# Kernel optimization log

Hardware: AMD Instinct MI355X
Metric: run time of the kernel (lower is better)

Reference implementation:

```python
import jax, jax.numpy as jnp
import numpy as np
from jax import lax

NEG = -1e30  # safe -inf surrogate (avoids inf-inf NaNs under vjp)


def setup_inputs() -> dict:
    key = jax.random.key(0)
    k1, k2, k3, k4 = jax.random.split(key, 4)
    B, T, U, V = 8, 128, 64, 1024
    acts = jax.random.normal(k1, (B, T, U + 1, V), dtype=jnp.float32)
    # labels in [1, V): blank (0) never appears in target sequences
    labels = jax.random.randint(k2, (B, U), 1, V, dtype=jnp.int32)
    act_lens = jax.random.randint(k3, (B,), T // 2, T + 1, dtype=jnp.int32)
    label_lens = jax.random.randint(k4, (B,), U // 2, U + 1, dtype=jnp.int32)
    return {"acts": acts, "labels": labels, "act_lens": act_lens, "label_lens": label_lens}


def _rnnt_costs(acts, labels, act_lens, label_lens, blank=0):
    """Per-example negative log-likelihood of the RNNT alignment lattice.
    acts: (B, T, U+1, V) logits (warp_rnnt applies log_softmax internally).
    """
    B, T, U1, V = acts.shape
    U = U1 - 1
    lp = jax.nn.log_softmax(acts, axis=-1)
    lp_blank = lp[..., blank]                                        # (B, T, U+1)
    lab = jnp.broadcast_to(labels[:, None, :, None], (B, T, U, 1))
    lp_label = jnp.take_along_axis(lp[:, :, :U, :], lab, axis=3)[..., 0]  # (B, T, U)
    # mask label emissions beyond each example's label length
    umask = jnp.arange(U)[None, :] < label_lens[:, None]             # (B, U)
    lp_label = jnp.where(umask[:, None, :], lp_label, NEG)

    def compute_row(fb, lt):
        # fb: (B, U+1) alpha[t-1, u] + lp_blank[t-1, u] (the "from below" term)
        # lt: (B, U)   label log-probs at time t
        # new[u] = logaddexp(fb[u], new[u-1] + lt[u-1])  -- sequential in u
        def u_step(carry, x):
            fb_u, lt_u = x
            new = jnp.logaddexp(fb_u, carry + lt_u)
            return new, new
        _, rest = lax.scan(u_step, fb[:, 0], (fb[:, 1:].T, lt.T))    # (U, B)
        return jnp.concatenate([fb[:, 0:1], rest.T], axis=1)         # (B, U+1)

    # t = 0 row: alpha[0,0] = 0; only label transitions along u
    fb0 = jnp.concatenate([jnp.zeros((B, 1), acts.dtype), jnp.full((B, U), NEG, acts.dtype)], axis=1)
    row0 = compute_row(fb0, lp_label[:, 0, :])

    def t_step(prev_row, x):
        lpb_prev, lt = x
        row = compute_row(prev_row + lpb_prev, lt)
        return row, row

    xs = (jnp.moveaxis(lp_blank[:, :-1, :], 0, 1),   # (T-1, B, U+1)
          jnp.moveaxis(lp_label[:, 1:, :], 0, 1))    # (T-1, B, U)
    _, rows = lax.scan(t_step, row0, xs)             # (T-1, B, U+1)
    alphas = jnp.concatenate([row0[None], rows], axis=0)  # (T, B, U+1)

    b = jnp.arange(B)
    tl = act_lens - 1
    final = alphas[tl, b, label_lens] + lp_blank[b, tl, label_lens]
    return -final                                     # (B,)


def reference(acts, labels, act_lens, label_lens):
    # matches torch module defaults: size_average=False, blank_label=0
    costs = _rnnt_costs(acts, labels, act_lens, label_lens, blank=0)
    return jnp.sum(costs).reshape(1)
```

## Files before the change

kernel.cpp:

```cpp
#include <hip/hip_runtime.h>

#define LN2F 0.6931471805599453f

#define B_   8
#define T_   128
#define U_   64
#define U1_  65
#define V_   1024
#define ROWS_ (B_*T_*U1_)
#define NDIAG_ 224
#define DS_    66
#define PACKB_ (NDIAG_*DS_)
#define COL0N_ 224
#define NWAVES_ 8192
#define K1_BLOCKS_ 2048

typedef float f32x4 __attribute__((ext_vector_type(4)));

__device__ __forceinline__ float shr1_f32(float x) {
  return __int_as_float(__builtin_amdgcn_update_dpp(
      0, __float_as_int(x), 0x138, 0xf, 0xf, true));
}

__device__ __forceinline__ float wave_fmax_dpp(float x) {
#define DPPM_(ctrl) { int t_ = __builtin_amdgcn_update_dpp(                  \
      __float_as_int(x), __float_as_int(x), (ctrl), 0xf, 0xf, false);        \
    x = fmaxf(x, __int_as_float(t_)); }
  DPPM_(0x111) DPPM_(0x112) DPPM_(0x114) DPPM_(0x118)
  DPPM_(0x142) DPPM_(0x143)
#undef DPPM_
  return __int_as_float(__builtin_amdgcn_readlane(__float_as_int(x), 63));
}

__device__ __forceinline__ float wave_fsum_dpp(float x) {
#define DPPA_(ctrl) { int t_ = __builtin_amdgcn_update_dpp(                  \
      0, __float_as_int(x), (ctrl), 0xf, 0xf, true);                         \
    x += __int_as_float(t_); }
  DPPA_(0x111) DPPA_(0x112) DPPA_(0x114) DPPA_(0x118)
  DPPA_(0x142) DPPA_(0x143)
#undef DPPA_
  return __int_as_float(__builtin_amdgcn_readlane(__float_as_int(x), 63));
}

__device__ __forceinline__ int wave_max_bexp(float a, float i0) {
  int e  = (int)((__float_as_uint(a)  >> 23) & 0xffu);
  int e2 = (int)((__float_as_uint(i0) >> 23) & 0xffu);
  e = max(e, e2);
  int t;
  t = __builtin_amdgcn_update_dpp(e, e, 0x111, 0xf, 0xf, false); e = max(e, t);
  t = __builtin_amdgcn_update_dpp(e, e, 0x112, 0xf, 0xf, false); e = max(e, t);
  t = __builtin_amdgcn_update_dpp(e, e, 0x114, 0xf, 0xf, false); e = max(e, t);
  t = __builtin_amdgcn_update_dpp(e, e, 0x118, 0xf, 0xf, false); e = max(e, t);
  t = __builtin_amdgcn_update_dpp(e, e, 0x142, 0xf, 0xf, false); e = max(e, t);
  t = __builtin_amdgcn_update_dpp(e, e, 0x143, 0xf, 0xf, false); e = max(e, t);
  return __builtin_amdgcn_readlane(e, 63);
}

__global__ __launch_bounds__(256) void k1_linsoftmax(
    const float* __restrict__ acts, const int* __restrict__ labels,
    const int* __restrict__ label_lens,
    float2* __restrict__ pack, float2* __restrict__ col0, int* __restrict__ cnt) {
  const int lane = threadIdx.x & 63;
  const int wid  = blockIdx.x * 4 + (threadIdx.x >> 6);
  if (wid == 0 && lane == 0) *cnt = 0;

  for (int row = wid; row < ROWS_; row += NWAVES_) {
    const int b   = row / (T_ * U1_);
    const int rem = row - b * (T_ * U1_);
    const int t   = rem / U1_;
    const int u   = rem - t * U1_;
    const float* __restrict__ p = acts + (size_t)row * V_;

    int ll_ = 0; float labv = 0.0f;
    if (lane == 0 && u < U_) {
      ll_  = label_lens[b];
      labv = p[labels[b * U_ + u]];
    }

    f32x4 v0 = *(const f32x4*)(p +   0 + lane * 4);
    f32x4 v1 = *(const f32x4*)(p + 256 + lane * 4);
    f32x4 v2 = *(const f32x4*)(p + 512 + lane * 4);
    f32x4 v3 = *(const f32x4*)(p + 768 + lane * 4);

    float ml = fmaxf(fmaxf(fmaxf(v0.x, v0.y), fmaxf(v0.z, v0.w)),
               fmaxf(fmaxf(fmaxf(v1.x, v1.y), fmaxf(v1.z, v1.w)),
               fmaxf(fmaxf(fmaxf(v2.x, v2.y), fmaxf(v2.z, v2.w)),
                     fmaxf(fmaxf(v3.x, v3.y), fmaxf(v3.z, v3.w)))));
    float m = wave_fmax_dpp(ml);

    float e00 = __expf(v0.x - m);
    float sl = e00          + __expf(v0.y - m) + __expf(v0.z - m) + __expf(v0.w - m)
             + __expf(v1.x - m) + __expf(v1.y - m) + __expf(v1.z - m) + __expf(v1.w - m)
             + __expf(v2.x - m) + __expf(v2.y - m) + __expf(v2.z - m) + __expf(v2.w - m)
             + __expf(v3.x - m) + __expf(v3.y - m) + __expf(v3.z - m) + __expf(v3.w - m);
    float s = wave_fsum_dpp(sl);

    if (lane == 0) {
      float rs = 1.0f / s;
      float pb = e00 * rs;
      float2* pk = pack + (size_t)b * PACKB_;
      if (u == 0) {
        float pl0 = __expf(labv - m) * rs;
        col0[b * COL0N_ + (t + 1)] = make_float2(pb, pl0);
        pk[(size_t)(t + 1) * DS_ + 1].x = pl0;
      } else {
        pk[(size_t)(t + u) * DS_ + u].y = pb;
        if (u < U_) {
          float plv = (u < ll_) ? (__expf(labv - m) * rs) : 0.0f;
          pk[(size_t)(t + u + 1) * DS_ + (u + 1)].x = plv;
        }
      }
    }
  }
}

__global__ __launch_bounds__(64) void k2_alpha(
    const float2* __restrict__ pack, const float2* __restrict__ col0,
    const int* __restrict__ act_lens, const int* __restrict__ label_lens,
    float* __restrict__ costs, int* __restrict__ cnt, float* __restrict__ out) {
  __shared__ float2 c0_s[COL0N_];
  const int b  = (int)blockIdx.x;
  const int l  = (int)threadIdx.x;

  {
    const float2* src = col0 + (size_t)b * COL0N_;
    #pragma unroll
    for (int k = 0; k < 4; ++k) {
      int i = k * 64 + l;
      if (i < COL0N_) {
        float2 v = src[i];
        bool ok = (i >= 1) && (i <= T_);
        c0_s[i] = ok ? v : make_float2(0.0f, 0.0f);
      }
    }
  }

  const int tl = act_lens[b] - 1;
  const int ll = label_lens[b];
  const int u  = l + 1;
  const int tcap = (u == ll) ? tl : 0x7fffffff;

  const float2* __restrict__ pku = pack + (size_t)b * PACKB_ + u;

  float a = 0.0f;
  float i0 = (l == 0) ? 1.0f : 0.0f;
  float fin = 0.0f, pbc = 0.0f;
  int   S = 0, Ecap = 0;
  int   t_ = -u;

  float2 pA[16], pB[16], pC[16], pD[16];
  float2 cA[16], cB[16], cC[16], cD[16];

#define LOADP(P, C, DB) do {                                             \
    const float2* q_ = pku + (size_t)(DB) * DS_;                         \
    _Pragma("unroll")                                                    \
    for (int j = 0; j < 16; ++j) (P)[j] = q_[(size_t)j * DS_];           \
    _Pragma("unroll")                                                    \
    for (int j = 0; j < 16; ++j) (C)[j] = c0_s[(DB) + j];                \
  } while (0)

#define RENORM() do {                                                    \
    int eS_ = wave_max_bexp(a, i0);                                      \
    int sh_ = min(167 - eS_, 126);     \
    S += sh_;                                                            \
    float sc_ = ldexpf(1.0f, sh_);                                       \
    a *= sc_; i0 *= sc_;                                                 \
  } while (0)

#define COMPUTE8(P, C, JO) do {                                          \
    _Pragma("unroll")                                                    \
    for (int jj = 0; jj < 8; ++jj) {                                     \
      const int j = (JO) + jj;                                           \
      t_ += 1;                                                           \
      float shin = shr1_f32(a);                                          \
      float inj  = i0 * (C)[j].y;                                        \
      float anew = fmaf(a, pbc, fmaf(shin, (P)[j].x, inj));              \
      bool valid = ((unsigned)t_ < (unsigned)T_);                        \
      a = valid ? anew : 0.0f;                \
      bool cap = (t_ == tcap);                                           \
      fin  = cap ? a : fin;                                              \
      Ecap = cap ? S : Ecap;                                             \
      i0 *= (C)[j].x;                                                    \
      pbc = (P)[j].y;                                                    \
    }                                                                    \
  } while (0)

  LOADP(pA, cA, 1);
  LOADP(pB, cB, 17);
  LOADP(pC, cC, 33);
  LOADP(pD, cD, 49);

  #pragma unroll 1
  for (int it4 = 0; it4 < 3; ++it4) {
    if (it4 > 0) RENORM();
    COMPUTE8(pA, cA, 0);
    RENORM();
    COMPUTE8(pA, cA, 8);
    if (it4 < 2) LOADP(pA, cA, 64 * it4 + 65);

    RENORM();
    COMPUTE8(pB, cB, 0);
    RENORM();
    COMPUTE8(pB, cB, 8);
    if (it4 < 2) LOADP(pB, cB, 64 * it4 + 81);

    RENORM();
    COMPUTE8(pC, cC, 0);
    RENORM();
    COMPUTE8(pC, cC, 8);
    if (it4 < 2) LOADP(pC, cC, 64 * it4 + 97);

    RENORM();
    COMPUTE8(pD, cD, 0);
    RENORM();
    COMPUTE8(pD, cD, 8);
    if (it4 < 2) LOADP(pD, cD, 64 * it4 + 113);
  }
#undef LOADP
#undef RENORM
#undef COMPUTE8

  if (u == ll) {
    float pblast = pack[(size_t)b * PACKB_ + (size_t)(tl + ll) * DS_ + ll].y;
    float lg = __log2f(fin) - (float)Ecap + __log2f(pblast);
    costs[b] = -lg * LN2F;
  }

  __threadfence();
  if (l == 0) {
    int old = atomicAdd(cnt, 1);
    if (old == B_ - 1) {
      __threadfence();
      volatile const float* vc = costs;
      float s = 0.0f;
      #pragma unroll
      for (int i = 0; i < B_; ++i) s += vc[i];
      out[0] = s;
    }
  }
}

extern "C" void kernel_launch(void* const* d_in, const int* in_sizes, int n_in,
                              void* d_out, int out_size, void* d_ws, size_t ws_size,
                              hipStream_t stream) {
  const float* acts       = (const float*)d_in[0];
  const int*   labels     = (const int*)d_in[1];
  const int*   act_lens   = (const int*)d_in[2];
  const int*   label_lens = (const int*)d_in[3];

  float2* pack  = (float2*)d_ws;
  float2* col0  = pack + (size_t)B_ * PACKB_;
  float*  costs = (float*)(col0 + (size_t)B_ * COL0N_);
  int*    cnt   = (int*)(costs + B_);

  k1_linsoftmax<<<K1_BLOCKS_, 256, 0, stream>>>(acts, labels, label_lens, pack, col0, cnt);
  k2_alpha<<<B_, 64, 0, stream>>>(pack, col0, act_lens, label_lens, costs, cnt, (float*)d_out);
}
```

Measured before the change: 57.34 us.

## Transpose packed lattice probs to per-lane rows in bf16 and prefetch all upfront

The lattice probability workspace is re-laid out so each lane's diagonal sequence is contiguous (one 256-entry row per u), and each label/blank pair is packed into a single 32-bit word of two bf16 values. The alpha kernel then issues all 13 groups of 16-byte vector loads up front instead of strided per-step float2 loads in four rotating buffers. This is meant to remove the latency-bound strided gathers on the single-wave serial recursion. The cost is lower precision (bf16 probabilities), which may change the loss beyond tolerance, and much higher register pressure.

```diff
diff --git a/kernel.cpp b/kernel.cpp
--- a/kernel.cpp
+++ b/kernel.cpp
@@ -8,9 +8,8 @@
 #define U1_  65
 #define V_   1024
 #define ROWS_ (B_*T_*U1_)
-#define NDIAG_ 224
-#define DS_    66
-#define PACKB_ (NDIAG_*DS_)
+#define PROW_ 256
+#define PACKT_B (64*PROW_)
 #define COL0N_ 224
 #define NWAVES_ 8192
 #define K1_BLOCKS_ 2048
@@ -56,10 +55,16 @@
   return __builtin_amdgcn_readlane(e, 63);
 }
 
+__device__ __forceinline__ unsigned short bf16_rn_(float f) {
+  unsigned b = __float_as_uint(f);
+  return (unsigned short)((b + 0x7fffu + ((b >> 16) & 1u)) >> 16);
+}
+
 __global__ __launch_bounds__(256) void k1_linsoftmax(
     const float* __restrict__ acts, const int* __restrict__ labels,
     const int* __restrict__ label_lens,
-    float2* __restrict__ pack, float2* __restrict__ col0, int* __restrict__ cnt) {
+    unsigned int* __restrict__ packT, float2* __restrict__ col0,
+    int* __restrict__ cnt) {
   const int lane = threadIdx.x & 63;
   const int wid  = blockIdx.x * 4 + (threadIdx.x >> 6);
   if (wid == 0 && lane == 0) *cnt = 0;
@@ -98,29 +103,29 @@
     if (lane == 0) {
       float rs = 1.0f / s;
       float pb = e00 * rs;
-      float2* pk = pack + (size_t)b * PACKB_;
+      unsigned int* pkb = packT + (size_t)b * PACKT_B;
       if (u == 0) {
         float pl0 = __expf(labv - m) * rs;
         col0[b * COL0N_ + (t + 1)] = make_float2(pb, pl0);
-        pk[(size_t)(t + 1) * DS_ + 1].x = pl0;
+        ((unsigned short*)(pkb + 0 * PROW_ + (t + 1)))[0] = bf16_rn_(pl0);
       } else {
-        pk[(size_t)(t + u) * DS_ + u].y = pb;
+        ((unsigned short*)(pkb + (u - 1) * PROW_ + (t + u)))[1] = bf16_rn_(pb);
         if (u < U_) {
           float plv = (u < ll_) ? (__expf(labv - m) * rs) : 0.0f;
-          pk[(size_t)(t + u + 1) * DS_ + (u + 1)].x = plv;
+          ((unsigned short*)(pkb + u * PROW_ + (t + u + 1)))[0] = bf16_rn_(plv);
         }
       }
     }
   }
 }
 
-__global__ __launch_bounds__(64) void k2_alpha(
-    const float2* __restrict__ pack, const float2* __restrict__ col0,
+__global__ __launch_bounds__(64, 1) void k2_alpha(
+    const unsigned int* __restrict__ packT, const float2* __restrict__ col0,
     const int* __restrict__ act_lens, const int* __restrict__ label_lens,
     float* __restrict__ costs, int* __restrict__ cnt, float* __restrict__ out) {
   __shared__ float2 c0_s[COL0N_];
-  const int b  = (int)blockIdx.x;
-  const int l  = (int)threadIdx.x;
+  const int b = (int)blockIdx.x;
+  const int l = (int)threadIdx.x;
 
   {
     const float2* src = col0 + (size_t)b * COL0N_;
@@ -129,8 +134,9 @@
       int i = k * 64 + l;
       if (i < COL0N_) {
         float2 v = src[i];
-        bool ok = (i >= 1) && (i <= T_);
-        c0_s[i] = ok ? v : make_float2(0.0f, 0.0f);
+        float2 z = make_float2(0.0f, 0.0f);
+        c0_s[i] = (i == 0) ? make_float2(1.0f, 0.0f)
+                           : ((i <= T_) ? v : z);
       }
     }
   }
@@ -138,90 +144,83 @@
   const int tl = act_lens[b] - 1;
   const int ll = label_lens[b];
   const int u  = l + 1;
-  const int tcap = (u == ll) ? tl : 0x7fffffff;
-
-  const float2* __restrict__ pku = pack + (size_t)b * PACKB_ + u;
+  const int dccap = (u == ll) ? (tl + u) : -1;
+
+  const uint4* __restrict__ rp =
+      (const uint4*)(packT + (size_t)b * PACKT_B + (size_t)l * PROW_);
+
+#define PF_(I) const uint4 q##I##_0 = rp[4*(I)+0], q##I##_1 = rp[4*(I)+1], \
+                           q##I##_2 = rp[4*(I)+2], q##I##_3 = rp[4*(I)+3];
+  PF_(0) PF_(1) PF_(2) PF_(3) PF_(4) PF_(5) PF_(6)
+  PF_(7) PF_(8) PF_(9) PF_(10) PF_(11) PF_(12)
+#undef PF_
 
   float a = 0.0f;
   float i0 = (l == 0) ? 1.0f : 0.0f;
   float fin = 0.0f, pbc = 0.0f;
   int   S = 0, Ecap = 0;
-  int   t_ = -u;
-
-  float2 pA[16], pB[16], pC[16], pD[16];
-  float2 cA[16], cB[16], cC[16], cD[16];
-
-#define LOADP(P, C, DB) do {                                             \
-    const float2* q_ = pku + (size_t)(DB) * DS_;                         \
-    _Pragma("unroll")                                                    \
-    for (int j = 0; j < 16; ++j) (P)[j] = q_[(size_t)j * DS_];           \
-    _Pragma("unroll")                                                    \
-    for (int j = 0; j < 16; ++j) (C)[j] = c0_s[(DB) + j];                \
-  } while (0)
-
-#define RENORM() do {                                                    \
+
+#define RENORM_() do {                                                   \
     int eS_ = wave_max_bexp(a, i0);                                      \
     int sh_ = min(167 - eS_, 126);     \
     S += sh_;                                                            \
     float sc_ = ldexpf(1.0f, sh_);                                       \
     a *= sc_; i0 *= sc_;                                                 \
-  } while (0)
-
-#define COMPUTE8(P, C, JO) do {                                          \
-    _Pragma("unroll")                                                    \
-    for (int jj = 0; jj < 8; ++jj) {                                     \
-      const int j = (JO) + jj;                                           \
-      t_ += 1;                                                           \
-      float shin = shr1_f32(a);                                          \
-      float inj  = i0 * (C)[j].y;                                        \
-      float anew = fmaf(a, pbc, fmaf(shin, (P)[j].x, inj));              \
-      bool valid = ((unsigned)t_ < (unsigned)T_);                        \
-      a = valid ? anew : 0.0f;                \
-      bool cap = (t_ == tcap);                                           \
-      fin  = cap ? a : fin;                                              \
-      Ecap = cap ? S : Ecap;                                             \
-      i0 *= (C)[j].x;                                                    \
-      pbc = (P)[j].y;                                                    \
-    }                                                                    \
-  } while (0)
-
-  LOADP(pA, cA, 1);
-  LOADP(pB, cB, 17);
-  LOADP(pC, cC, 33);
-  LOADP(pD, cD, 49);
-
-  #pragma unroll 1
-  for (int it4 = 0; it4 < 3; ++it4) {
-    if (it4 > 0) RENORM();
-    COMPUTE8(pA, cA, 0);
-    RENORM();
-    COMPUTE8(pA, cA, 8);
-    if (it4 < 2) LOADP(pA, cA, 64 * it4 + 65);
-
-    RENORM();
-    COMPUTE8(pB, cB, 0);
-    RENORM();
-    COMPUTE8(pB, cB, 8);
-    if (it4 < 2) LOADP(pB, cB, 64 * it4 + 81);
-
-    RENORM();
-    COMPUTE8(pC, cC, 0);
-    RENORM();
-    COMPUTE8(pC, cC, 8);
-    if (it4 < 2) LOADP(pC, cC, 64 * it4 + 97);
-
-    RENORM();
-    COMPUTE8(pD, cD, 0);
-    RENORM();
-    COMPUTE8(pD, cD, 8);
-    if (it4 < 2) LOADP(pD, cD, 64 * it4 + 113);
-  }
-#undef LOADP
-#undef RENORM
-#undef COMPUTE8
+  } while (0);
+
+#define STEP_(DC, VV, CC) do {                                           \
+    const unsigned int v_ = (VV);                                        \
+    float shin = shr1_f32(a);                                            \
+    float inj  = i0 * (CC).y;                                            \
+    float anew = fmaf(a, pbc,                                            \
+                      fmaf(shin, __uint_as_float(v_ << 16), inj));       \
+    bool valid = (u <= (DC)) && (u + T_ > (DC));       \
+    a = valid ? anew : 0.0f;                                             \
+    bool cap = (dccap == (DC));                                          \
+    fin  = cap ? a : fin;                                                \
+    Ecap = cap ? S : Ecap;                                               \
+    i0 *= (CC).x;                                                        \
+    pbc = __uint_as_float(v_ & 0xffff0000u);                             \
+  } while (0);
+
+#define BURST_(DC0, Q0, Q1, Q2, Q3, C)                                   \
+  RENORM_()                                                              \
+  STEP_((DC0)+0,  (Q0).x, (C)[0])  STEP_((DC0)+1,  (Q0).y, (C)[1])       \
+  STEP_((DC0)+2,  (Q0).z, (C)[2])  STEP_((DC0)+3,  (Q0).w, (C)[3])       \
+  STEP_((DC0)+4,  (Q1).x, (C)[4])  STEP_((DC0)+5,  (Q1).y, (C)[5])       \
+  STEP_((DC0)+6,  (Q1).z, (C)[6])  STEP_((DC0)+7,  (Q1).w, (C)[7])       \
+  RENORM_()                                                              \
+  STEP_((DC0)+8,  (Q2).x, (C)[8])  STEP_((DC0)+9,  (Q2).y, (C)[9])       \
+  STEP_((DC0)+10, (Q2).z, (C)[10]) STEP_((DC0)+11, (Q2).w, (C)[11])      \
+  STEP_((DC0)+12, (Q3).x, (C)[12]) STEP_((DC0)+13, (Q3).y, (C)[13])      \
+  STEP_((DC0)+14, (Q3).z, (C)[14]) STEP_((DC0)+15, (Q3).w, (C)[15])
+
+#define LOADC_(C, DC0) { _Pragma("unroll")                               \
+    for (int j_ = 0; j_ < 16; ++j_) (C)[j_] = c0_s[(DC0) + j_]; }
+
+  float2 cA[16], cB[16];
+  LOADC_(cA, 0); LOADC_(cB, 16);
+  BURST_(0,   q0_0,  q0_1,  q0_2,  q0_3,  cA) LOADC_(cA, 32);
+  BURST_(16,  q1_0,  q1_1,  q1_2,  q1_3,  cB) LOADC_(cB, 48);
+  BURST_(32,  q2_0,  q2_1,  q2_2,  q2_3,  cA) LOADC_(cA, 64);
+  BURST_(48,  q3_0,  q3_1,  q3_2,  q3_3,  cB) LOADC_(cB, 80);
+  BURST_(64,  q4_0,  q4_1,  q4_2,  q4_3,  cA) LOADC_(cA, 96);
+  BURST_(80,  q5_0,  q5_1,  q5_2,  q5_3,  cB) LOADC_(cB, 112);
+  BURST_(96,  q6_0,  q6_1,  q6_2,  q6_3,  cA) LOADC_(cA, 128);
+  BURST_(112, q7_0,  q7_1,  q7_2,  q7_3,  cB) LOADC_(cB, 144);
+  BURST_(128, q8_0,  q8_1,  q8_2,  q8_3,  cA) LOADC_(cA, 160);
+  BURST_(144, q9_0,  q9_1,  q9_2,  q9_3,  cB) LOADC_(cB, 176);
+  BURST_(160, q10_0, q10_1, q10_2, q10_3, cA) LOADC_(cA, 192);
+  BURST_(176, q11_0, q11_1, q11_2, q11_3, cB)
+  BURST_(192, q12_0, q12_1, q12_2, q12_3, cA)
+#undef BURST_
+#undef STEP_
+#undef RENORM_
+#undef LOADC_
 
   if (u == ll) {
-    float pblast = pack[(size_t)b * PACKB_ + (size_t)(tl + ll) * DS_ + ll].y;
+    unsigned int vlast = packT[(size_t)b * PACKT_B + (size_t)(ll - 1) * PROW_ + (tl + ll)];
+    float pblast = __uint_as_float(vlast & 0xffff0000u);
     float lg = __log2f(fin) - (float)Ecap + __log2f(pblast);
     costs[b] = -lg * LN2F;
   }
@@ -248,11 +247,11 @@
   const int*   act_lens   = (const int*)d_in[2];
   const int*   label_lens = (const int*)d_in[3];
 
-  float2* pack  = (float2*)d_ws;
-  float2* col0  = pack + (size_t)B_ * PACKB_;
+  unsigned int* packT = (unsigned int*)d_ws;
+  float2* col0  = (float2*)(packT + (size_t)B_ * PACKT_B);
   float*  costs = (float*)(col0 + (size_t)B_ * COL0N_);
   int*    cnt   = (int*)(costs + B_);
 
-  k1_linsoftmax<<<K1_BLOCKS_, 256, 0, stream>>>(acts, labels, label_lens, pack, col0, cnt);
-  k2_alpha<<<B_, 64, 0, stream>>>(pack, col0, act_lens, label_lens, costs, cnt, (float*)d_out);
-}
+  k1_linsoftmax<<<K1_BLOCKS_, 256, 0, stream>>>(acts, labels, label_lens, packT, col0, cnt);
+  k2_alpha<<<B_, 64, 0, stream>>>(packT, col0, act_lens, label_lens, costs, cnt, (float*)d_out);
+}
```

Measured after the change: 61.64 us. +7.5%, slower.
